# Optimization experiments

Measured on AMD Instinct MI355X. Metric: run time of the kernel, lower is better.

The kernel has to match this reference:

```python
import jax, jax.numpy as jnp
import numpy as np

DEPTH = 6
N_LEAF = 2 ** DEPTH          # 64
GATE_COUNT = N_LEAF - 1      # 63
B = 1024
GATING_FEATURES = 512
IN_FEATURES = 512
OUT_FEATURES = 512


def setup_inputs() -> dict:
    key = jax.random.key(0)
    k1, k2, k3, k4 = jax.random.split(key, 4)
    x_gating = jax.random.normal(k1, (B, GATING_FEATURES), dtype=jnp.float32)
    x_leaf = jax.random.normal(k2, (B, IN_FEATURES), dtype=jnp.float32)
    # kaiming-normal-ish init scales
    gw = jax.random.normal(k3, (GATING_FEATURES, GATE_COUNT), dtype=jnp.float32) * (1.0 / np.sqrt(GATING_FEATURES))
    gb = jnp.zeros((GATE_COUNT,), dtype=jnp.float32)
    pw = jax.random.normal(k4, (OUT_FEATURES, IN_FEATURES, N_LEAF), dtype=jnp.float32) * (1.0 / np.sqrt(IN_FEATURES))
    pb = jnp.zeros((OUT_FEATURES, N_LEAF), dtype=jnp.float32)
    return {"x_gating": x_gating, "x_leaf": x_leaf, "gw": gw, "gb": gb, "pw": pw, "pb": pb}


def _leaf_probs(x_gating, gw, gb):
    # gatings: (B, gate_count), internal nodes in breadth-first order
    gatings = jax.nn.sigmoid(x_gating @ gw + gb)
    b = gatings.shape[0]
    dens = jnp.ones((b, 1), dtype=gatings.dtype)  # root density
    start = 0
    for d in range(DEPTH):
        n_par = 2 ** d
        g = gatings[:, start:start + n_par]          # (B, n_par)
        # left child (even it+1) gets g, right child gets 1-g, interleaved
        dens = jnp.stack([dens * g, dens * (1.0 - g)], axis=-1).reshape(b, 2 * n_par)
        start += n_par
    return dens  # (B, n_leaf) = leaf densities (last n_leaf node densities)


def reference(x_gating, x_leaf, gw, gb, pw, pb):
    leaf_probs = _leaf_probs(x_gating, gw, gb)              # (B, L)
    # gated projection applied to x_leaf, summed over leaves:
    # equals ((pw @ leaf_probs.T).permute(2,0,1) @ x_leaf[...,None])[...,0]
    result = jnp.einsum('oil,bl,bi->bo', pw, leaf_probs, x_leaf)
    result = result + leaf_probs @ pb.T                     # gated bias (B, O)
    return result
```

## Files before the change

### kernel.cpp

```cpp
#include <hip/hip_runtime.h>
#include <stdint.h>

#define B_SZ   1024
#define GF     512
#define GC     63
#define NLEAF  64
#define IN_F   512
#define OUT_F  512

typedef float f32x4 __attribute__((ext_vector_type(4)));
typedef __fp16 h16x2 __attribute__((ext_vector_type(2)));
typedef __fp16 h16x8 __attribute__((ext_vector_type(8)));
typedef _Float16 f16x2 __attribute__((ext_vector_type(2)));

union HF8 { f16x2 h2[4]; h16x8 v; uint4 u; };

__device__ inline f16x2 pkrtz(float a, float b) {
  union { h16x2 r; f16x2 f; } u;
  u.r = __builtin_amdgcn_cvt_pkrtz(a, b);
  return u.f;
}

__global__ __launch_bounds__(512, 2) void k_leafprobs(
    const float* __restrict__ xg, const float* __restrict__ gw,
    const float* __restrict__ gb, float* __restrict__ p_ws)
{
  __shared__ float xsr[GF];
  __shared__ float part[512];
  __shared__ float gates[GC + 1];
  const int b = blockIdx.x;
  const int t = threadIdx.x;

  xsr[t] = xg[(size_t)b * GF + t];
  __syncthreads();

  const int ks = t >> 6, g = t & 63;
  float acc = 0.f;
  if (g < GC) {
    const float* gp = gw + (size_t)(ks * 64) * GC + g;
    const float* xp = &xsr[ks * 64];
#pragma unroll 8
    for (int k = 0; k < 64; ++k) acc += xp[k] * gp[(size_t)k * GC];
  }
  part[t] = acc;
  __syncthreads();

  if (t < GC) {
    float s = gb[t];
#pragma unroll
    for (int r = 0; r < 8; ++r) s += part[r * 64 + t];
    gates[t] = 1.f / (1.f + expf(-s));
  }
  __syncthreads();

  if (t < NLEAF) {
    float v = 1.f;
    int idx = 0, start = 0;
#pragma unroll
    for (int d = 0; d < 6; ++d) {
      int bit = (t >> (5 - d)) & 1;
      float gg = gates[start + idx];
      v *= bit ? (1.f - gg) : gg;
      idx = 2 * idx + bit;
      start += (1 << d);
    }
    p_ws[(size_t)b * NLEAF + t] = v;
  }
}

#define SK 16
#define KI 32

template <bool ATOMIC>
__global__ __launch_bounds__(256, 2) void k_fused(
    const float* __restrict__ x_leaf,
    const float* __restrict__ p_ws,
    const float* __restrict__ pw,
    float* __restrict__ dst)
{
  __shared__ __align__(16) float         xs[KI][256];
  __shared__ __align__(16) unsigned char bs8[2 * 8192];

  const int tid  = threadIdx.x;
  const int lane = tid & 63;
  const int wid  = tid >> 6;
  const int quad = lane >> 4;
  const int l15  = lane & 15;
  const int l7   = l15 & 7;

  const int bid = blockIdx.x;
  const int nt  = bid & 7;
  const int mt  = (bid >> 3) & 3;
  const int kc  = bid >> 5;

  const int row_m0 = mt * 256;
  const int o0     = nt * 64;
  const int i0     = kc * KI;
  const int wm     = wid * 64;

  {
    const float* src = x_leaf + (size_t)(row_m0 + tid) * IN_F + i0;
#pragma unroll
    for (int q = 0; q < 8; ++q) {
      float4 v = *(const float4*)(src + q * 4);
      xs[q * 4 + 0][tid] = v.x;
      xs[q * 4 + 1][tid] = v.y;
      xs[q * 4 + 2][tid] = v.z;
      xs[q * 4 + 3][tid] = v.w;
    }
  }

  HF8 prh[4][2];
#pragma unroll
  for (int mi = 0; mi < 4; ++mi) {
    const int row = row_m0 + wm + mi * 16 + l15;
#pragma unroll
    for (int ks = 0; ks < 2; ++ks) {
      const f32x4* src = (const f32x4*)(p_ws + (size_t)row * NLEAF + ks * 32 + quad * 8);
      f32x4 lo = src[0], hi = src[1];
      prh[mi][ks].h2[0] = pkrtz(lo[0], lo[1]);
      prh[mi][ks].h2[1] = pkrtz(lo[2], lo[3]);
      prh[mi][ks].h2[2] = pkrtz(hi[0], hi[1]);
      prh[mi][ks].h2[3] = pkrtz(hi[2], hi[3]);
    }
  }

  const int br  = tid >> 2;
  const int seg = tid & 3;
  const float* bsrc0 = pw + ((size_t)(o0 + br) * IN_F + i0) * NLEAF + seg * 16;

  const int wsw   = (br & 7) << 4;
  const int woff0 = br * 128 + ((seg * 32) ^ wsw);
  const int woff1 = br * 128 + ((seg * 32 + 16) ^ wsw);
  int coff[2];
#pragma unroll
  for (int ks = 0; ks < 2; ++ks)
    coff[ks] = (ks * 64 + quad * 16) ^ (l7 << 4);
  const int rbase = l15 * 128;

  f32x4 acc[4][4];
#pragma unroll
  for (int mi = 0; mi < 4; ++mi)
#pragma unroll
    for (int ni = 0; ni < 4; ++ni)
      acc[mi][ni] = (f32x4)(0.f);

  f32x4 rb[4][4];

#define BLOAD(T, SLOT)                                                        \
  {                                                                           \
    const float* a_ = bsrc0 + (size_t)(T) * NLEAF;                            \
    asm volatile(                                                             \
        "global_load_dwordx4 %0, %4, off\n\t"                                 \
        "global_load_dwordx4 %1, %4, off offset:16\n\t"                       \
        "global_load_dwordx4 %2, %4, off offset:32\n\t"                       \
        "global_load_dwordx4 %3, %4, off offset:48"                           \
        : "=v"(rb[SLOT][0]), "=v"(rb[SLOT][1]),                               \
          "=v"(rb[SLOT][2]), "=v"(rb[SLOT][3])                                \
        : "v"(a_));                                                           \
  }

#define BWAIT_(SLOT, N)                                                       \
  asm volatile("s_waitcnt vmcnt(" #N ")"                                      \
               : "+v"(rb[SLOT][0]), "+v"(rb[SLOT][1]),                        \
                 "+v"(rb[SLOT][2]), "+v"(rb[SLOT][3])::"memory");             \
  __builtin_amdgcn_sched_barrier(0);
#define BWAIT(SLOT, N) BWAIT_(SLOT, N)

#define BSTAGE(SLOT, BUF)                                                     \
  {                                                                           \
    HF8 c0_, c1_;                                                             \
    f32x4 a0_ = rb[SLOT][0], a1_ = rb[SLOT][1];                               \
    f32x4 a2_ = rb[SLOT][2], a3_ = rb[SLOT][3];                               \
    c0_.h2[0] = pkrtz(a0_[0], a0_[1]);                                        \
    c0_.h2[1] = pkrtz(a0_[2], a0_[3]);                                        \
    c0_.h2[2] = pkrtz(a1_[0], a1_[1]);                                        \
    c0_.h2[3] = pkrtz(a1_[2], a1_[3]);                                        \
    c1_.h2[0] = pkrtz(a2_[0], a2_[1]);                                        \
    c1_.h2[1] = pkrtz(a2_[2], a2_[3]);                                        \
    c1_.h2[2] = pkrtz(a3_[0], a3_[1]);                                        \
    c1_.h2[3] = pkrtz(a3_[2], a3_[3]);                                        \
    *(uint4*)(bs8 + (BUF) * 8192 + woff0) = c0_.u;                            \
    *(uint4*)(bs8 + (BUF) * 8192 + woff1) = c1_.u;                            \
  }

#define BARRIER() asm volatile("s_waitcnt lgkmcnt(0)\n\ts_barrier" ::: "memory")

#define COMPUTE(IT, BUF)                                                      \
  {                                                                           \
    float xvf[4];                                                             \
    _Float16 xh[4];                                                           \
    _Pragma("unroll")                                                         \
    for (int mi = 0; mi < 4; ++mi) xvf[mi] = xs[(IT)][wm + mi * 16 + l15];    \
    _Pragma("unroll")                                                         \
    for (int mi = 0; mi < 4; ++mi) xh[mi] = (_Float16)xvf[mi];                \
    const unsigned char* bsr_ = bs8 + (BUF) * 8192;                           \
    __builtin_amdgcn_s_setprio(1);                                            \
    _Pragma("unroll")                                                         \
    for (int ks = 0; ks < 2; ++ks) {                                          \
      h16x8 af[4];                                                            \
      _Pragma("unroll")                                                       \
      for (int mi = 0; mi < 4; ++mi) {                                        \
        HF8 t_;                                                               \
        f16x2 xp_; xp_[0] = xh[mi]; xp_[1] = xh[mi];                          \
        _Pragma("unroll")                                                     \
        for (int j = 0; j < 4; ++j) t_.h2[j] = prh[mi][ks].h2[j] * xp_;       \
        af[mi] = t_.v;                                                        \
      }                                                                       \
      _Pragma("unroll")                                                       \
      for (int ni = 0; ni < 4; ++ni) {                                        \
        h16x8 bfr = *(const h16x8*)(bsr_ + ni * 2048 + rbase + coff[ks]);     \
        _Pragma("unroll")                                                     \
        for (int mi = 0; mi < 4; ++mi)                                        \
          acc[mi][ni] = __builtin_amdgcn_mfma_f32_16x16x32_f16(               \
              af[mi], bfr, acc[mi][ni], 0, 0, 0);                             \
      }                                                                       \
    }                                                                         \
    __builtin_amdgcn_s_setprio(0);                                            \
  }

#define STEP(IT, BUF, SNX, WN, DL)                                            \
  {                                                                           \
    COMPUTE(IT, BUF)                                                          \
    BWAIT(SNX, WN)                                                            \
    BSTAGE(SNX, (BUF) ^ 1)                                                    \
    if (DL) { BLOAD((IT) + 5, SNX) }                                          \
    BARRIER();                                                                \
  }

  BLOAD(0, 0)
  BLOAD(1, 1)
  BLOAD(2, 2)
  BLOAD(3, 3)
  BWAIT(0, 12)
  BSTAGE(0, 0)
  BLOAD(4, 0)
  BARRIER();

  for (int itb = 0; itb < 24; itb += 4) {
    STEP(itb + 0, 0, 1, 12, 1)
    STEP(itb + 1, 1, 2, 12, 1)
    STEP(itb + 2, 0, 3, 12, 1)
    STEP(itb + 3, 1, 0, 12, 1)
  }
  STEP(24, 0, 1, 12, 1)
  STEP(25, 1, 2, 12, 1)
  STEP(26, 0, 3, 12, 1)
  STEP(27, 1, 0, 12, 0)
  STEP(28, 0, 1, 8, 0)
  STEP(29, 1, 2, 4, 0)
  STEP(30, 0, 3, 0, 0)
  COMPUTE(31, 1)

#undef BLOAD
#undef BWAIT
#undef BWAIT_
#undef BSTAGE
#undef BARRIER
#undef COMPUTE
#undef STEP

#pragma unroll
  for (int mi = 0; mi < 4; ++mi) {
#pragma unroll
    for (int ni = 0; ni < 4; ++ni) {
      int row = row_m0 + wm + mi * 16 + quad * 4;
      int col = o0 + ni * 16 + l15;
      if (ATOMIC) {
        float* o = dst + (size_t)row * OUT_F + col;
        atomicAdd(o,             acc[mi][ni][0]);
        atomicAdd(o + OUT_F,     acc[mi][ni][1]);
        atomicAdd(o + 2 * OUT_F, acc[mi][ni][2]);
        atomicAdd(o + 3 * OUT_F, acc[mi][ni][3]);
      } else {
        float* o = dst + ((size_t)kc << 19) + (size_t)row * OUT_F + col;
        o[0]         = acc[mi][ni][0];
        o[OUT_F]     = acc[mi][ni][1];
        o[2 * OUT_F] = acc[mi][ni][2];
        o[3 * OUT_F] = acc[mi][ni][3];
      }
    }
  }
}

__global__ __launch_bounds__(256, 4) void k_reduce(
    const float* __restrict__ parts, const float* __restrict__ p_ws,
    const float* __restrict__ pb, float* __restrict__ out, int nparts)
{
  __shared__ float ps_l[2 * NLEAF];
  const int t  = threadIdx.x;
  const int b0 = blockIdx.x * 2;

  if (t < 32)
    ((f32x4*)ps_l)[t] = ((const f32x4*)(p_ws + (size_t)b0 * NLEAF))[t];
  __syncthreads();

  const int row = b0 + (t >> 7);
  const int c0  = (t & 127) * 4;
  const f32x4* ps = (const f32x4*)&ps_l[(t >> 7) * NLEAF];

  f32x4 a;
#pragma unroll
  for (int jo = 0; jo < 4; ++jo) {
    const f32x4* pbo = (const f32x4*)(pb + (size_t)(c0 + jo) * NLEAF);
    f32x4 s = (f32x4)(0.f);
#pragma unroll
    for (int lv = 0; lv < 16; ++lv) s += pbo[lv] * ps[lv];
    a[jo] = s[0] + s[1] + s[2] + s[3];
  }

#pragma unroll 8
  for (int k = 0; k < nparts; ++k)
    a += *(const f32x4*)(parts + ((size_t)k << 19) + (size_t)row * OUT_F + c0);

  *(f32x4*)(out + (size_t)row * OUT_F + c0) = a;
}

extern "C" void kernel_launch(void* const* d_in, const int* in_sizes, int n_in,
                              void* d_out, int out_size, void* d_ws, size_t ws_size,
                              hipStream_t stream) {
  const float* xg = (const float*)d_in[0];
  const float* xl = (const float*)d_in[1];
  const float* gw = (const float*)d_in[2];
  const float* gb = (const float*)d_in[3];
  const float* pw = (const float*)d_in[4];
  const float* pb = (const float*)d_in[5];
  float* out = (float*)d_out;

  const size_t P_BYTES = (size_t)B_SZ * NLEAF * 4;
  const size_t SLICE   = (size_t)B_SZ * OUT_F * 4;

  float* p_ws  = (float*)d_ws;
  float* parts = (float*)((char*)d_ws + P_BYTES);

  k_leafprobs<<<dim3(B_SZ), dim3(512), 0, stream>>>(xg, gw, gb, p_ws);

  if (ws_size >= P_BYTES + SK * SLICE) {
    k_fused<false><<<dim3(512), dim3(256), 0, stream>>>(xl, p_ws, pw, parts);
    k_reduce<<<dim3(512), dim3(256), 0, stream>>>(parts, p_ws, pb, out, SK);
  } else {
    k_reduce<<<dim3(512), dim3(256), 0, stream>>>(parts, p_ws, pb, out, 0);
    k_fused<true><<<dim3(512), dim3(256), 0, stream>>>(xl, p_ws, pw, out);
  }
}
```

Baseline: 166.3 us.

## Stage two k-iterations per LDS buffer to halve barriers in pipeline

Measured after the change: 166.5 us. No clear change (+0.1%).

```diff
diff --git a/kernel.cpp b/kernel.cpp
--- a/kernel.cpp
+++ b/kernel.cpp
@@ -79,7 +79,7 @@
     float* __restrict__ dst)
 {
   __shared__ __align__(16) float         xs[KI][256];
-  __shared__ __align__(16) unsigned char bs8[2 * 8192];
+  __shared__ __align__(16) unsigned char bs8[2 * 16384];
 
   const int tid  = threadIdx.x;
   const int lane = tid & 63;
@@ -155,9 +155,9 @@
         "global_load_dwordx4 %1, %4, off offset:16\n\t"                       \
         "global_load_dwordx4 %2, %4, off offset:32\n\t"                       \
         "global_load_dwordx4 %3, %4, off offset:48"                           \
-        : "=v"(rb[SLOT][0]), "=v"(rb[SLOT][1]),                               \
-          "=v"(rb[SLOT][2]), "=v"(rb[SLOT][3])                                \
-        : "v"(a_));                                                           \
+        : "=&v"(rb[SLOT][0]), "=&v"(rb[SLOT][1]),                             \
+          "=&v"(rb[SLOT][2]), "=&v"(rb[SLOT][3])                              \
+        : "v"(a_) : "memory");                                                \
   }
 
 #define BWAIT_(SLOT, N)                                                       \
@@ -167,7 +167,7 @@
   __builtin_amdgcn_sched_barrier(0);
 #define BWAIT(SLOT, N) BWAIT_(SLOT, N)
 
-#define BSTAGE(SLOT, BUF)                                                     \
+#define BSTAGE(SLOT, BUF, SUB)                                                \
   {                                                                           \
     HF8 c0_, c1_;                                                             \
     f32x4 a0_ = rb[SLOT][0], a1_ = rb[SLOT][1];                               \
@@ -180,13 +180,14 @@
     c1_.h2[1] = pkrtz(a2_[2], a2_[3]);                                        \
     c1_.h2[2] = pkrtz(a3_[0], a3_[1]);                                        \
     c1_.h2[3] = pkrtz(a3_[2], a3_[3]);                                        \
-    *(uint4*)(bs8 + (BUF) * 8192 + woff0) = c0_.u;                            \
-    *(uint4*)(bs8 + (BUF) * 8192 + woff1) = c1_.u;                            \
+    unsigned char* d_ = bs8 + (BUF) * 16384 + (SUB) * 8192;                   \
+    *(uint4*)(d_ + woff0) = c0_.u;                                            \
+    *(uint4*)(d_ + woff1) = c1_.u;                                            \
   }
 
 #define BARRIER() asm volatile("s_waitcnt lgkmcnt(0)\n\ts_barrier" ::: "memory")
 
-#define COMPUTE(IT, BUF)                                                      \
+#define COMPUTE(IT, BUF, SUB)                                                 \
   {                                                                           \
     float xvf[4];                                                             \
     _Float16 xh[4];                                                           \
@@ -194,7 +195,7 @@
     for (int mi = 0; mi < 4; ++mi) xvf[mi] = xs[(IT)][wm + mi * 16 + l15];    \
     _Pragma("unroll")                                                         \
     for (int mi = 0; mi < 4; ++mi) xh[mi] = (_Float16)xvf[mi];                \
-    const unsigned char* bsr_ = bs8 + (BUF) * 8192;                           \
+    const unsigned char* bsr_ = bs8 + (BUF) * 16384 + (SUB) * 8192;           \
     __builtin_amdgcn_s_setprio(1);                                            \
     _Pragma("unroll")                                                         \
     for (int ks = 0; ks < 2; ++ks) {                                          \
@@ -219,12 +220,16 @@
     __builtin_amdgcn_s_setprio(0);                                            \
   }
 
-#define STEP(IT, BUF, SNX, WN, DL)                                            \
+#define PHASE(IT0, BUF, SA, SB, WA, WB, DLA, DLB)                             \
   {                                                                           \
-    COMPUTE(IT, BUF)                                                          \
-    BWAIT(SNX, WN)                                                            \
-    BSTAGE(SNX, (BUF) ^ 1)                                                    \
-    if (DL) { BLOAD((IT) + 5, SNX) }                                          \
+    COMPUTE(IT0, BUF, 0)                                                      \
+    BWAIT(SA, WA)                                                             \
+    BSTAGE(SA, (BUF) ^ 1, 0)                                                  \
+    if (DLA) { BLOAD((IT0) + 6, SA) }                                         \
+    COMPUTE((IT0) + 1, BUF, 1)                                                \
+    BWAIT(SB, WB)                                                             \
+    BSTAGE(SB, (BUF) ^ 1, 1)                                                  \
+    if (DLB) { BLOAD((IT0) + 7, SB) }                                         \
     BARRIER();                                                                \
   }
 
@@ -233,24 +238,24 @@
   BLOAD(2, 2)
   BLOAD(3, 3)
   BWAIT(0, 12)
-  BSTAGE(0, 0)
+  BSTAGE(0, 0, 0)
+  BWAIT(1, 8)
+  BSTAGE(1, 0, 1)
   BLOAD(4, 0)
+  BLOAD(5, 1)
   BARRIER();
 
-  for (int itb = 0; itb < 24; itb += 4) {
-    STEP(itb + 0, 0, 1, 12, 1)
-    STEP(itb + 1, 1, 2, 12, 1)
-    STEP(itb + 2, 0, 3, 12, 1)
-    STEP(itb + 3, 1, 0, 12, 1)
-  }
-  STEP(24, 0, 1, 12, 1)
-  STEP(25, 1, 2, 12, 1)
-  STEP(26, 0, 3, 12, 1)
-  STEP(27, 1, 0, 12, 0)
-  STEP(28, 0, 1, 8, 0)
-  STEP(29, 1, 2, 4, 0)
-  STEP(30, 0, 3, 0, 0)
-  COMPUTE(31, 1)
+  for (int pp = 0; pp < 24; pp += 8) {
+    PHASE(pp + 0, 0, 2, 3, 12, 12, 1, 1)
+    PHASE(pp + 2, 1, 0, 1, 12, 12, 1, 1)
+    PHASE(pp + 4, 0, 2, 3, 12, 12, 1, 1)
+    PHASE(pp + 6, 1, 0, 1, 12, 12, 1, 1)
+  }
+  PHASE(24, 0, 2, 3, 12, 12, 1, 1)
+  PHASE(26, 1, 0, 1, 12, 8, 0, 0)
+  PHASE(28, 0, 2, 3, 4, 0, 0, 0)
+  COMPUTE(30, 1, 0)
+  COMPUTE(31, 1, 1)
 
 #undef BLOAD
 #undef BWAIT
@@ -258,7 +263,7 @@
 #undef BSTAGE
 #undef BARRIER
 #undef COMPUTE
-#undef STEP
+#undef PHASE
 
 #pragma unroll
   for (int mi = 0; mi < 4; ++mi) {
```
